# Optimization experiments

Hardware: AMD Instinct MI355X
Metric: run time of the kernel (lower is better)

The kernel has to match this reference:

```python
import jax, jax.numpy as jnp
import numpy as np

B, L, D, N = 4, 1024, 1024, 16
HD = D // N
DFF = 4 * D
EPS = 1e-5


def _ln(x, g, b):
    m = jnp.mean(x, axis=-1, keepdims=True)
    v = jnp.mean(jnp.square(x - m), axis=-1, keepdims=True)
    return (x - m) * jax.lax.rsqrt(v + EPS) * g + b


def setup_inputs() -> dict:
    key = jax.random.key(0)
    ks = jax.random.split(key, 8)
    s = 0.02
    return {
        "x": jax.random.normal(ks[0], (B, L, D), jnp.float32),
        "decay": jax.random.uniform(ks[1], (N, L, L), jnp.float32),
        "ln1_g": jnp.ones((D,), jnp.float32),
        "ln1_b": jnp.zeros((D,), jnp.float32),
        "proj_W": jax.random.normal(ks[2], (4 * D, D), jnp.float32) * s,
        "proj_b": jnp.zeros((4 * D,), jnp.float32),
        "reto_W": jax.random.normal(ks[3], (D, D), jnp.float32) * s,
        "reto_b": jnp.zeros((D,), jnp.float32),
        "ln2_g": jnp.ones((D,), jnp.float32),
        "ln2_b": jnp.zeros((D,), jnp.float32),
        "ffn1_W": jax.random.normal(ks[4], (DFF, D), jnp.float32) * s,
        "ffn1_b": jnp.zeros((DFF,), jnp.float32),
        "ffn2_W": jax.random.normal(ks[5], (D, DFF), jnp.float32) * s,
        "ffn2_b": jnp.zeros((D,), jnp.float32),
    }


def reference(x, decay, ln1_g, ln1_b, proj_W, proj_b, reto_W, reto_b,
              ln2_g, ln2_b, ffn1_W, ffn1_b, ffn2_W, ffn2_b):
    ln_x = _ln(x, ln1_g, ln1_b)
    p = ln_x @ proj_W.T + proj_b                      # [B, L, 4D]
    q, k, v, xo = jnp.split(p, 4, axis=-1)            # each [B, L, D]

    def heads(t):  # [B, L, D] -> [B, N, L, HD]
        return t.reshape(B, L, N, HD).transpose(0, 2, 1, 3)

    q, k, v = heads(q), heads(k), heads(v)
    scores = jnp.einsum('bnld,bnmd->bnlm', q, k) * decay[None]  # [B,N,L,L]
    ret = jnp.einsum('bnlm,bnmd->bnld', scores, v)              # [B,N,L,HD]
    ret = ret.transpose(0, 2, 1, 3).reshape(B, L, D)
    ret = ret * jax.nn.silu(xo)                                  # gated
    ret = ret @ reto_W.T + reto_b
    x = x + ret
    h = _ln(x, ln2_g, ln2_b)
    h = jax.nn.gelu(h @ ffn1_W.T + ffn1_b, approximate=False) @ ffn2_W.T + ffn2_b
    return x + h
```

## Files before the change

kernel.cpp:

```cpp
#include <hip/hip_runtime.h>


typedef _Float16 f16;
typedef _Float16 f16x8 __attribute__((ext_vector_type(8)));
typedef float floatx4 __attribute__((ext_vector_type(4)));

#define EP_BIAS_F16      0
#define EP_DECAY_F16     1
#define EP_BIAS_GELU_F16 2
#define EP_PARTIAL_F32   3

template <bool F32> struct out_sel { typedef f16 T; };
template <> struct out_sel<true>   { typedef float T; };

__device__ __forceinline__ void gload_lds16(const void* g, void* s) {
    __builtin_amdgcn_global_load_lds(
        (const __attribute__((address_space(1))) unsigned int*)g,
        (__attribute__((address_space(3))) unsigned int*)s, 16, 0, 0);
}

__device__ __forceinline__ float erf_fast(float x) {
    const float ax = fabsf(x);
    const float t  = __builtin_amdgcn_rcpf(1.f + 0.3275911f * ax);
    const float p  = t * (0.254829592f + t * (-0.284496736f + t * (1.421413741f +
                     t * (-1.453152027f + t * 1.061405429f))));
    const float r  = 1.f - p * __expf(-ax * ax);
    return copysignf(r, x);
}

__global__ __launch_bounds__(256, 2) void attn_fused(
    const f16* __restrict__ p, const f16* __restrict__ vT,
    const float* __restrict__ decay, f16* __restrict__ gated)
{
    const int y  = blockIdx.y;
    const int bp = y >> 4, h = y & 15;
    const int m0 = blockIdx.x * 64;

    __shared__ __align__(16) f16 Kb[4][64 * 64];
    __shared__ __align__(16) f16 Vb[4][64 * 64];
    __shared__ __align__(16) f16 Ss[4][16 * 68];

    const int t    = threadIdx.x;
    const int lane = t & 63;
    const int w    = t >> 6;
    const int quad = lane >> 4;
    const int fr   = lane & 15;
    const int wq0  = w * 16;

    const int b0 = bp * 2, b1 = b0 + 1;
    const int z0 = b0 * 16 + h, z1 = z0 + 16;
    const f16*   Qg0 = p + ((size_t)h * 4096 + b0 * 1024 + m0) * 64;
    const f16*   Qg1 = p + ((size_t)h * 4096 + b1 * 1024 + m0) * 64;
    const f16*   Kg0 = p + ((size_t)(16 + h) * 4096 + b0 * 1024) * 64;
    const f16*   Kg1 = p + ((size_t)(16 + h) * 4096 + b1 * 1024) * 64;
    const f16*   Vg0 = vT + (size_t)z0 * 65536;
    const f16*   Vg1 = vT + (size_t)z1 * 65536;
    const f16*   XOg0 = p + ((size_t)(48 + h) * 4096 + b0 * 1024 + m0) * 64;
    const f16*   XOg1 = p + ((size_t)(48 + h) * 4096 + b1 * 1024 + m0) * 64;
    const float* Dg  = decay + (size_t)h * 1048576 + (size_t)m0 * 1024;

    f16x8 q00, q01, q10, q11;
    {
        const size_t qrow = (size_t)(wq0 + fr) * 64;
        q00 = *(const f16x8*)(Qg0 + qrow + (0 * 4 + quad) * 8);
        q01 = *(const f16x8*)(Qg0 + qrow + (1 * 4 + quad) * 8);
        q10 = *(const f16x8*)(Qg1 + qrow + (0 * 4 + quad) * 8);
        q11 = *(const f16x8*)(Qg1 + qrow + (1 * 4 + quad) * 8);
    }

    floatx4 oa0[4] = {}, oa1[4] = {};
    float dA[16], dB[16];

    const float* Dt = Dg + (size_t)(wq0 + quad * 4) * 1024 + fr;

#define DLOAD(dst, jj) { _Pragma("unroll") \
    for (int tn = 0; tn < 4; ++tn) { _Pragma("unroll") \
      for (int r = 0; r < 4; ++r) \
        dst[tn * 4 + r] = Dt[(size_t)r * 1024 + (jj) + tn * 16]; } \
    __builtin_amdgcn_sched_barrier(0); }

#define STAGE(Kgp, Vgp, jj, pb) { _Pragma("unroll") \
    for (int i_ = 0; i_ < 2; ++i_) { \
      const int ci = t + i_ * 256; \
      const int r_ = ci >> 3; \
      const int c_ = ((ci & 7) ^ (r_ & 7)) * 8; \
      gload_lds16((Kgp) + (size_t)(jj) * 64 + r_ * 64 + c_, &Kb[pb][ci * 8]); \
      gload_lds16((Vgp) + (size_t)(jj) * 64 + r_ * 64 + c_, &Vb[pb][ci * 8]); \
    } }

#define VMBAR(N) { asm volatile("s_waitcnt vmcnt(" #N ")" ::: "memory"); \
    __builtin_amdgcn_s_barrier(); __builtin_amdgcn_sched_barrier(0); }

#define STEP(qa, qb, oa, dreg, pb) { \
    floatx4 sa[4] = {}; \
    _Pragma("unroll") \
    for (int kc = 0; kc < 2; ++kc) { \
      const int cc = kc * 4 + quad; \
      f16x8 bf[4]; \
      _Pragma("unroll") \
      for (int tn = 0; tn < 4; ++tn) { \
        const int kv = tn * 16 + fr; \
        bf[tn] = *(const f16x8*)&Kb[pb][(kv * 8 + (cc ^ (kv & 7))) * 8]; \
      } \
      _Pragma("unroll") \
      for (int tn = 0; tn < 4; ++tn) \
        sa[tn] = __builtin_amdgcn_mfma_f32_16x16x32_f16(kc ? (qb) : (qa), bf[tn], sa[tn], 0, 0, 0); \
    } \
    _Pragma("unroll") \
    for (int tn = 0; tn < 4; ++tn) { _Pragma("unroll") \
      for (int r = 0; r < 4; ++r) \
        Ss[w][(quad * 4 + r) * 68 + tn * 16 + fr] = (f16)(sa[tn][r] * dreg[tn * 4 + r]); } \
    _Pragma("unroll") \
    for (int kc = 0; kc < 2; ++kc) { \
      const int cc = kc * 4 + quad; \
      const f16x8 af = *(const f16x8*)&Ss[w][fr * 68 + cc * 8]; \
      f16x8 bf[4]; \
      _Pragma("unroll") \
      for (int tn = 0; tn < 4; ++tn) { \
        const int d = tn * 16 + fr; \
        bf[tn] = *(const f16x8*)&Vb[pb][(d * 8 + (cc ^ (d & 7))) * 8]; \
      } \
      _Pragma("unroll") \
      for (int tn = 0; tn < 4; ++tn) \
        oa[tn] = __builtin_amdgcn_mfma_f32_16x16x32_f16(af, bf[tn], oa[tn], 0, 0, 0); \
    } }

#define EPILOG(oa, XOgp, bq) { \
    _Pragma("unroll") \
    for (int tn = 0; tn < 4; ++tn) { _Pragma("unroll") \
      for (int r = 0; r < 4; ++r) { \
        const int qrow = wq0 + quad * 4 + r; \
        const int d = tn * 16 + fr; \
        float g = (float)XOgp[(size_t)qrow * 64 + d]; \
        g = g * __builtin_amdgcn_rcpf(1.f + __expf(-g)); \
        Ss[w][(quad * 4 + r) * 68 + tn * 16 + fr] = (f16)(oa[tn][r] * g); \
      } } \
    f16* Og = gated + (size_t)((bq) * 1024 + m0 + wq0) * 1024 + h * 64; \
    _Pragma("unroll") \
    for (int i = 0; i < 2; ++i) { \
      const int jj = lane + i * 64; \
      const int rr = jj >> 3; \
      const int cc = jj & 7; \
      const uint2 lo = *(const uint2*)&Ss[w][rr * 68 + cc * 8]; \
      const uint2 hi = *(const uint2*)&Ss[w][rr * 68 + cc * 8 + 4]; \
      uint4 val = make_uint4(lo.x, lo.y, hi.x, hi.y); \
      *(uint4*)(Og + (size_t)rr * 1024 + cc * 8) = val; \
    } }

    DLOAD(dA, 0);
    STAGE(Kg0, Vg0, 0, 0);
    STAGE(Kg1, Vg1, 0, 1);
    VMBAR(4);

    for (int i = 0; i < 7; ++i) {
        const int j1 = i * 128 + 64;
        const int j2 = i * 128 + 128;
        DLOAD(dB, j1);
        STAGE(Kg0, Vg0, j1, 2);
        STEP(q00, q01, oa0, dA, 0);
        VMBAR(4);
        STAGE(Kg1, Vg1, j1, 3);
        STEP(q10, q11, oa1, dA, 1);
        VMBAR(4);
        DLOAD(dA, j2);
        STAGE(Kg0, Vg0, j2, 0);
        STEP(q00, q01, oa0, dB, 2);
        VMBAR(4);
        STAGE(Kg1, Vg1, j2, 1);
        STEP(q10, q11, oa1, dB, 3);
        VMBAR(4);
    }
    {
        DLOAD(dB, 960);
        STAGE(Kg0, Vg0, 960, 2);
        STEP(q00, q01, oa0, dA, 0);
        VMBAR(4);
        STAGE(Kg1, Vg1, 960, 3);
        STEP(q10, q11, oa1, dA, 1);
        VMBAR(4);
        STEP(q00, q01, oa0, dB, 2);
        VMBAR(0);
        STEP(q10, q11, oa1, dB, 3);
    }

    EPILOG(oa0, XOg0, b0);
    EPILOG(oa1, XOg1, b1);

#undef DLOAD
#undef STAGE
#undef VMBAR
#undef STEP
#undef EPILOG
}

template <int BM, int BN, int WM, int WN, int EP, int XSWZ, int PTILED = 0>
__global__ __launch_bounds__(256, 4) void gemm_bt(
    const f16* __restrict__ A, const f16* __restrict__ B, void* __restrict__ Cv,
    int M, int N, int K, int lda, int ldb, int ldc,
    long long sAo, long long sAi, long long sBo, long long sBi,
    long long sCo, long long sCi, int inner,
    int nsplit, int Kc, long long sCk,
    const float* __restrict__ bias,
    const void* __restrict__ aux, long long sXo, long long sXi, int ldaux)
{
    constexpr bool OUT_F32 = (EP == EP_PARTIAL_F32);
    typedef typename out_sel<OUT_F32>::T OutT;
    constexpr int ESIZE       = OUT_F32 ? 4 : 2;
    constexpr int CSTRIDE     = BN + 4;
    constexpr int TILE_BYTES  = (BM + BN) * 64 * 2;
    constexpr int STAGE_BYTES = OUT_F32 ? 0 : BM * CSTRIDE * ESIZE;
    constexpr int SMEM_BYTES  = TILE_BYTES > STAGE_BYTES ? TILE_BYTES : STAGE_BYTES;

    __shared__ __align__(16) char smem[SMEM_BYTES];
    f16*  As = (f16*)smem;
    f16*  Bs = (f16*)(smem + BM * 128);
    OutT* Cs = (OutT*)smem;

    int z = blockIdx.z;
    const int ks = z % nsplit; z /= nsplit;
    const int zo = z / inner, zi = z % inner;
    A += zo * sAo + zi * sAi;
    B += zo * sBo + zi * sBi;
    const long long cOff = (long long)zo * sCo + (long long)zi * sCi + (long long)ks * sCk;
    const long long xOff = (long long)zo * sXo + (long long)zi * sXi;

    int bx = blockIdx.x, by = blockIdx.y;
    if constexpr (XSWZ) {
        const int gx  = gridDim.x;
        const int nb  = gx * gridDim.y;
        const int lin = bx + gx * by;
        const int nlin = (lin & 7) * (nb >> 3) + (lin >> 3);
        bx = nlin % gx;
        by = nlin / gx;
    }
    const int m0 = by * BM;
    const int n0 = bx * BN;

    const int t    = threadIdx.x;
    const int lane = t & 63;
    const int w    = t >> 6;
    const int wm   = (w >> 1) * (WM * 16);
    const int wn   = (w & 1) * (WN * 16);
    const int fr   = lane & 15;
    const int quad = lane >> 4;

    constexpr int ACH = BM / 32;
    constexpr int BCH = BN / 32;

    floatx4 acc[WM][WN] = {};

    const int kbeg = ks * Kc, kend = kbeg + Kc;
    for (int kk = kbeg; kk < kend; kk += 64) {
#pragma unroll
        for (int i = 0; i < ACH; ++i) {
            const int ci = t + i * 256;
            const int r  = ci >> 3;
            const int c  = ((ci & 7) ^ (r & 7)) * 8;
            gload_lds16(A + (size_t)(m0 + r) * lda + kk + c, &As[ci * 8]);
        }
#pragma unroll
        for (int i = 0; i < BCH; ++i) {
            const int ci = t + i * 256;
            const int r  = ci >> 3;
            const int c  = ((ci & 7) ^ (r & 7)) * 8;
            gload_lds16(B + (size_t)(n0 + r) * ldb + kk + c, &Bs[ci * 8]);
        }
        __syncthreads();

#pragma unroll
        for (int kh = 0; kh < 2; ++kh) {
            const int cc = kh * 4 + quad;
            f16x8 af[WM], bf[WN];
#pragma unroll
            for (int tm = 0; tm < WM; ++tm) {
                const int r = wm + tm * 16 + fr;
                af[tm] = *(const f16x8*)&As[(r * 8 + (cc ^ (r & 7))) * 8];
            }
#pragma unroll
            for (int tn = 0; tn < WN; ++tn) {
                const int r = wn + tn * 16 + fr;
                bf[tn] = *(const f16x8*)&Bs[(r * 8 + (cc ^ (r & 7))) * 8];
            }
#pragma unroll
            for (int tm = 0; tm < WM; ++tm)
#pragma unroll
                for (int tn = 0; tn < WN; ++tn)
                    acc[tm][tn] = __builtin_amdgcn_mfma_f32_16x16x32_f16(af[tm], bf[tn], acc[tm][tn], 0, 0, 0);
        }
        __syncthreads();
    }

    const int er = quad * 4;
    const int ec = lane & 15;
    if constexpr (OUT_F32) {
        float* Pg = (float*)Cv + cOff;
#pragma unroll
        for (int tm = 0; tm < WM; ++tm)
#pragma unroll
            for (int tn = 0; tn < WN; ++tn)
#pragma unroll
                for (int r = 0; r < 4; ++r) {
                    const int grow = m0 + wm + tm * 16 + er + r;
                    const int gcol = n0 + wn + tn * 16 + ec;
                    Pg[(size_t)grow * ldc + gcol] = acc[tm][tn][r];
                }
        return;
    }

#pragma unroll
    for (int tm = 0; tm < WM; ++tm) {
#pragma unroll
        for (int tn = 0; tn < WN; ++tn) {
#pragma unroll
            for (int r = 0; r < 4; ++r) {
                const int lrow = wm + tm * 16 + er + r;
                const int col  = wn + tn * 16 + ec;
                const int grow = m0 + lrow;
                const int gcol = n0 + col;
                const float v = acc[tm][tn][r];
                float val;
                if constexpr (EP == EP_BIAS_F16) {
                    val = v + bias[gcol];
                } else if constexpr (EP == EP_DECAY_F16) {
                    const float* dk = (const float*)aux + xOff;
                    val = v * dk[(size_t)grow * ldaux + gcol];
                } else if constexpr (EP == EP_BIAS_GELU_F16) {
                    const float u = v + bias[gcol];
                    val = 0.5f * u * (1.f + erf_fast(u * 0.70710678118f));
                } else {
                    val = v;
                }
                Cs[lrow * CSTRIDE + col] = (OutT)val;
            }
        }
    }
    __syncthreads();

    constexpr int PER_ROW = BN * ESIZE / 16;
    constexpr int NCHUNK  = (BM * PER_ROW) / 256;
#pragma unroll
    for (int i = 0; i < NCHUNK; ++i) {
        const int j  = t + i * 256;
        const int rr = j / PER_ROW;
        const int cc = j - rr * PER_ROW;
        const char* src = smem + (size_t)rr * (CSTRIDE * ESIZE) + (size_t)cc * 16;
        const uint2 lo = *(const uint2*)src;
        const uint2 hi = *(const uint2*)(src + 8);
        uint4 val = make_uint4(lo.x, lo.y, hi.x, hi.y);
        char* dst;
        if constexpr (PTILED) {
            const int gc0 = n0 + cc * 8;
            dst = (char*)Cv +
                (((size_t)(gc0 >> 6) * 4096 + (m0 + rr)) * 64 + (gc0 & 63)) * 2;
        } else {
            dst = (char*)Cv +
                (size_t)(cOff + (long long)(m0 + rr) * ldc + n0) * ESIZE +
                (size_t)cc * 16;
        }
        *(uint4*)dst = val;
    }
}

__global__ __launch_bounds__(256) void reduce2_bias_res(
    const float4* __restrict__ P, const float* __restrict__ bias,
    const float4* __restrict__ res, float4* __restrict__ out)
{
    const int i = blockIdx.x * 256 + threadIdx.x;
    const int col4 = i & 255;
    const float4 a = P[i];
    const float4 b = P[i + 1048576];
    const float4 r = res[i];
    const float4 bi = ((const float4*)bias)[col4];
    float4 o;
    o.x = a.x + b.x + r.x + bi.x;
    o.y = a.y + b.y + r.y + bi.y;
    o.z = a.z + b.z + r.z + bi.z;
    o.w = a.w + b.w + r.w + bi.w;
    out[i] = o;
}

__global__ __launch_bounds__(256) void ln_to_f16(
    const float* __restrict__ x, const float* __restrict__ g,
    const float* __restrict__ b, f16* __restrict__ out)
{
    const int row = blockIdx.x;
    const int t = threadIdx.x;
    const float4 xv = ((const float4*)(x + (size_t)row * 1024))[t];
    float s  = xv.x + xv.y + xv.z + xv.w;
    float ss = xv.x * xv.x + xv.y * xv.y + xv.z * xv.z + xv.w * xv.w;
    for (int o = 32; o > 0; o >>= 1) {
        s  += __shfl_down(s, o, 64);
        ss += __shfl_down(ss, o, 64);
    }
    __shared__ float red[8];
    const int wv = t >> 6;
    if ((t & 63) == 0) { red[wv] = s; red[wv + 4] = ss; }
    __syncthreads();
    s  = red[0] + red[1] + red[2] + red[3];
    ss = red[4] + red[5] + red[6] + red[7];
    const float mean = s * (1.f / 1024.f);
    const float var  = ss * (1.f / 1024.f) - mean * mean;
    const float rstd = rsqrtf(var + 1e-5f);
    const float4 gv = ((const float4*)g)[t];
    const float4 bv = ((const float4*)b)[t];
    alignas(8) f16 h[4];
    h[0] = (f16)((xv.x - mean) * rstd * gv.x + bv.x);
    h[1] = (f16)((xv.y - mean) * rstd * gv.y + bv.y);
    h[2] = (f16)((xv.z - mean) * rstd * gv.z + bv.z);
    h[3] = (f16)((xv.w - mean) * rstd * gv.w + bv.w);
    ((uint2*)(out + (size_t)row * 1024))[t] = *(uint2*)h;
}

__global__ __launch_bounds__(256) void cast_f32_f16(
    const float* __restrict__ in, f16* __restrict__ out, int n4)
{
    const int i = blockIdx.x * 256 + threadIdx.x;
    if (i < n4) {
        const float4 v = ((const float4*)in)[i];
        alignas(8) f16 h[4] = {(f16)v.x, (f16)v.y, (f16)v.z, (f16)v.w};
        ((uint2*)out)[i] = *(uint2*)h;
    }
}

__global__ __launch_bounds__(256) void transpose_v(
    const f16* __restrict__ p, f16* __restrict__ vT)
{
    const int z = blockIdx.y;
    const int b = z >> 4, h = z & 15;
    const int m0 = blockIdx.x * 64;
    __shared__ f16 tile[64][72];
    const int t = threadIdx.x;
    const f16* src = p + ((size_t)(32 + h) * 4096 + b * 1024 + m0) * 64;
#pragma unroll
    for (int pass = 0; pass < 4; ++pass) {
        const int r = (t >> 4) + pass * 16;
        const int c = (t & 15) * 4;
        *(uint2*)&tile[r][c] = *(const uint2*)(src + (size_t)r * 64 + c);
    }
    __syncthreads();
    f16* dst = vT + (size_t)z * 65536 + (size_t)(m0 >> 6) * 4096;
#pragma unroll
    for (int pass = 0; pass < 4; ++pass) {
        const int d  = (t >> 4) + pass * 16;
        const int mc = (t & 15) * 4;
        alignas(8) f16 tmp[4] = {tile[mc][d], tile[mc + 1][d], tile[mc + 2][d], tile[mc + 3][d]};
        *(uint2*)(dst + (size_t)d * 64 + mc) = *(uint2*)tmp;
    }
}

extern "C" void kernel_launch(void* const* d_in, const int* in_sizes, int n_in,
                              void* d_out, int out_size, void* d_ws, size_t ws_size,
                              hipStream_t stream) {
    const float* x      = (const float*)d_in[0];
    const float* decay  = (const float*)d_in[1];
    const float* ln1_g  = (const float*)d_in[2];
    const float* ln1_b  = (const float*)d_in[3];
    const float* proj_W = (const float*)d_in[4];
    const float* proj_b = (const float*)d_in[5];
    const float* reto_W = (const float*)d_in[6];
    const float* reto_b = (const float*)d_in[7];
    const float* ln2_g  = (const float*)d_in[8];
    const float* ln2_b  = (const float*)d_in[9];
    const float* ffn1_W = (const float*)d_in[10];
    const float* ffn1_b = (const float*)d_in[11];
    const float* ffn2_W = (const float*)d_in[12];
    const float* ffn2_b = (const float*)d_in[13];
    float* out = (float*)d_out;

    char* w = (char*)d_ws;
    auto alloc = [&](size_t bytes) { char* r = w; w += (bytes + 255) & ~(size_t)255; return r; };
    f16*   Wp   = (f16*)alloc((size_t)4096 * 1024 * 2);
    f16*   Wr   = (f16*)alloc((size_t)1024 * 1024 * 2);
    f16*   W1   = (f16*)alloc((size_t)4096 * 1024 * 2);
    f16*   W2   = (f16*)alloc((size_t)1024 * 4096 * 2);
    f16*   buf8 = (f16*)alloc((size_t)4096 * 1024 * 2);
    f16*   p    = (f16*)alloc((size_t)4096 * 4096 * 2);
    f16*   S    = (f16*)alloc((size_t)16 * 1024 * 1024 * 2);
    float* y    = (float*)alloc((size_t)4096 * 1024 * 4);

    f16*   lnx   = buf8;
    f16*   vT    = buf8;
    f16*   hln   = buf8;
    f16*   gated = Wp;
    f16*   ffh   = p;
    float* Pk    = (float*)S;

    cast_f32_f16<<<4096, 256, 0, stream>>>(proj_W, Wp, 1048576);
    cast_f32_f16<<<1024, 256, 0, stream>>>(reto_W, Wr, 262144);
    cast_f32_f16<<<4096, 256, 0, stream>>>(ffn1_W, W1, 1048576);
    cast_f32_f16<<<4096, 256, 0, stream>>>(ffn2_W, W2, 1048576);

    ln_to_f16<<<4096, 256, 0, stream>>>(x, ln1_g, ln1_b, lnx);

    gemm_bt<128, 128, 4, 4, EP_BIAS_F16, 1, 1><<<dim3(32, 32, 1), 256, 0, stream>>>(
        lnx, Wp, p, 4096, 4096, 1024, 1024, 1024, 4096,
        0, 0, 0, 0, 0, 0, 1, 1, 1024, 0, proj_b, nullptr, 0, 0, 0);

    transpose_v<<<dim3(16, 64), 256, 0, stream>>>(p, vT);

    attn_fused<<<dim3(16, 32), 256, 0, stream>>>(p, vT, decay, gated);

    gemm_bt<128, 128, 4, 4, EP_PARTIAL_F32, 1><<<dim3(8, 32, 2), 256, 0, stream>>>(
        gated, Wr, Pk, 4096, 1024, 1024, 1024, 1024, 1024,
        0, 0, 0, 0, 0, 0, 1, 2, 512, 4194304, nullptr, nullptr, 0, 0, 0);
    reduce2_bias_res<<<4096, 256, 0, stream>>>(
        (const float4*)Pk, reto_b, (const float4*)x, (float4*)y);

    ln_to_f16<<<4096, 256, 0, stream>>>(y, ln2_g, ln2_b, hln);

    gemm_bt<128, 128, 4, 4, EP_BIAS_GELU_F16, 1><<<dim3(32, 32, 1), 256, 0, stream>>>(
        hln, W1, ffh, 4096, 4096, 1024, 1024, 1024, 4096,
        0, 0, 0, 0, 0, 0, 1, 1, 1024, 0, ffn1_b, nullptr, 0, 0, 0);

    gemm_bt<128, 128, 4, 4, EP_PARTIAL_F32, 1><<<dim3(8, 32, 2), 256, 0, stream>>>(
        ffh, W2, Pk, 4096, 1024, 4096, 4096, 4096, 1024,
        0, 0, 0, 0, 0, 0, 1, 2, 2048, 4194304, nullptr, nullptr, 0, 0, 0);
    reduce2_bias_res<<<4096, 256, 0, stream>>>(
        (const float4*)Pk, ffn2_b, (const float4*)y, (float4*)out);
}
```

Baseline: 390.8 us.

## Widen attention blocks to 128 queries with triple-buffered shared K/V tiles

The retention attention kernel now runs 512 threads per block and covers 128 query rows per block instead of 64, so each staged K/V tile in LDS serves eight waves. Global and L2 traffic for K and V drops accordingly. Staging moves from a four-slot ping-pong to a three-stage ring that loads both batches' K/V together, which needs one barrier per step instead of two. The grid halves and each CU holds one large block using about 113KB of LDS rather than two smaller ones. That makes load imbalance across CUs and latency hiding within a single block the main risks.

```diff
diff --git a/kernel.cpp b/kernel.cpp
--- a/kernel.cpp
+++ b/kernel.cpp
@@ -28,17 +28,17 @@
     return copysignf(r, x);
 }
 
-__global__ __launch_bounds__(256, 2) void attn_fused(
+__global__ __launch_bounds__(512, 1) void attn_fused(
     const f16* __restrict__ p, const f16* __restrict__ vT,
     const float* __restrict__ decay, f16* __restrict__ gated)
 {
     const int y  = blockIdx.y;
     const int bp = y >> 4, h = y & 15;
-    const int m0 = blockIdx.x * 64;
-
-    __shared__ __align__(16) f16 Kb[4][64 * 64];
-    __shared__ __align__(16) f16 Vb[4][64 * 64];
-    __shared__ __align__(16) f16 Ss[4][16 * 68];
+    const int m0 = blockIdx.x * 128;
+
+    __shared__ __align__(16) f16 Kb[3][2][64 * 64];
+    __shared__ __align__(16) f16 Vb[3][2][64 * 64];
+    __shared__ __align__(16) f16 Ss[8][16 * 68];
 
     const int t    = threadIdx.x;
     const int lane = t & 63;
@@ -57,7 +57,6 @@
     const f16*   Vg1 = vT + (size_t)z1 * 65536;
     const f16*   XOg0 = p + ((size_t)(48 + h) * 4096 + b0 * 1024 + m0) * 64;
     const f16*   XOg1 = p + ((size_t)(48 + h) * 4096 + b1 * 1024 + m0) * 64;
-    const float* Dg  = decay + (size_t)h * 1048576 + (size_t)m0 * 1024;
 
     f16x8 q00, q01, q10, q11;
     {
@@ -71,7 +70,8 @@
     floatx4 oa0[4] = {}, oa1[4] = {};
     float dA[16], dB[16];
 
-    const float* Dt = Dg + (size_t)(wq0 + quad * 4) * 1024 + fr;
+    const float* Dt = decay + (size_t)h * 1048576
+                    + (size_t)(m0 + wq0 + quad * 4) * 1024 + fr;
 
 #define DLOAD(dst, jj) { _Pragma("unroll") \
     for (int tn = 0; tn < 4; ++tn) { _Pragma("unroll") \
@@ -79,19 +79,19 @@
         dst[tn * 4 + r] = Dt[(size_t)r * 1024 + (jj) + tn * 16]; } \
     __builtin_amdgcn_sched_barrier(0); }
 
-#define STAGE(Kgp, Vgp, jj, pb) { _Pragma("unroll") \
-    for (int i_ = 0; i_ < 2; ++i_) { \
-      const int ci = t + i_ * 256; \
-      const int r_ = ci >> 3; \
-      const int c_ = ((ci & 7) ^ (r_ & 7)) * 8; \
-      gload_lds16((Kgp) + (size_t)(jj) * 64 + r_ * 64 + c_, &Kb[pb][ci * 8]); \
-      gload_lds16((Vgp) + (size_t)(jj) * 64 + r_ * 64 + c_, &Vb[pb][ci * 8]); \
-    } }
+#define STAGE2(jj, pb) { \
+    const int r_ = t >> 3; \
+    const int c_ = ((t & 7) ^ (r_ & 7)) * 8; \
+    const size_t go_ = (size_t)(jj) * 64 + r_ * 64 + c_; \
+    gload_lds16(Kg0 + go_, &Kb[pb][0][t * 8]); \
+    gload_lds16(Vg0 + go_, &Vb[pb][0][t * 8]); \
+    gload_lds16(Kg1 + go_, &Kb[pb][1][t * 8]); \
+    gload_lds16(Vg1 + go_, &Vb[pb][1][t * 8]); }
 
 #define VMBAR(N) { asm volatile("s_waitcnt vmcnt(" #N ")" ::: "memory"); \
     __builtin_amdgcn_s_barrier(); __builtin_amdgcn_sched_barrier(0); }
 
-#define STEP(qa, qb, oa, dreg, pb) { \
+#define STEPB(qa, qb, oa, dreg, kb, vb) { \
     floatx4 sa[4] = {}; \
     _Pragma("unroll") \
     for (int kc = 0; kc < 2; ++kc) { \
@@ -100,7 +100,7 @@
       _Pragma("unroll") \
       for (int tn = 0; tn < 4; ++tn) { \
         const int kv = tn * 16 + fr; \
-        bf[tn] = *(const f16x8*)&Kb[pb][(kv * 8 + (cc ^ (kv & 7))) * 8]; \
+        bf[tn] = *(const f16x8*)&(kb)[(kv * 8 + (cc ^ (kv & 7))) * 8]; \
       } \
       _Pragma("unroll") \
       for (int tn = 0; tn < 4; ++tn) \
@@ -118,7 +118,7 @@
       _Pragma("unroll") \
       for (int tn = 0; tn < 4; ++tn) { \
         const int d = tn * 16 + fr; \
-        bf[tn] = *(const f16x8*)&Vb[pb][(d * 8 + (cc ^ (d & 7))) * 8]; \
+        bf[tn] = *(const f16x8*)&(vb)[(d * 8 + (cc ^ (d & 7))) * 8]; \
       } \
       _Pragma("unroll") \
       for (int tn = 0; tn < 4; ++tn) \
@@ -147,50 +147,48 @@
       *(uint4*)(Og + (size_t)rr * 1024 + cc * 8) = val; \
     } }
 
+#define MSTEP(pb, dcur, dnxt, jnext, jstage) { \
+    DLOAD(dnxt, jnext); \
+    STAGE2(jstage, (pb + 2) % 3); \
+    STEPB(q00, q01, oa0, dcur, Kb[pb][0], Vb[pb][0]); \
+    STEPB(q10, q11, oa1, dcur, Kb[pb][1], Vb[pb][1]); \
+    VMBAR(4); }
+
     DLOAD(dA, 0);
-    STAGE(Kg0, Vg0, 0, 0);
-    STAGE(Kg1, Vg1, 0, 1);
+    STAGE2(0, 0);
+    STAGE2(64, 1);
     VMBAR(4);
 
-    for (int i = 0; i < 7; ++i) {
-        const int j1 = i * 128 + 64;
-        const int j2 = i * 128 + 128;
-        DLOAD(dB, j1);
-        STAGE(Kg0, Vg0, j1, 2);
-        STEP(q00, q01, oa0, dA, 0);
-        VMBAR(4);
-        STAGE(Kg1, Vg1, j1, 3);
-        STEP(q10, q11, oa1, dA, 1);
-        VMBAR(4);
-        DLOAD(dA, j2);
-        STAGE(Kg0, Vg0, j2, 0);
-        STEP(q00, q01, oa0, dB, 2);
-        VMBAR(4);
-        STAGE(Kg1, Vg1, j2, 1);
-        STEP(q10, q11, oa1, dB, 3);
-        VMBAR(4);
-    }
+#pragma unroll
+    for (int i = 0; i < 2; ++i) {
+        const int j0 = i * 384;
+        MSTEP(0, dA, dB, j0 + 64,  j0 + 128);
+        MSTEP(1, dB, dA, j0 + 128, j0 + 192);
+        MSTEP(2, dA, dB, j0 + 192, j0 + 256);
+        MSTEP(0, dB, dA, j0 + 256, j0 + 320);
+        MSTEP(1, dA, dB, j0 + 320, j0 + 384);
+        MSTEP(2, dB, dA, j0 + 384, j0 + 448);
+    }
+    MSTEP(0, dA, dB, 832, 896);
+    MSTEP(1, dB, dA, 896, 960);
     {
         DLOAD(dB, 960);
-        STAGE(Kg0, Vg0, 960, 2);
-        STEP(q00, q01, oa0, dA, 0);
-        VMBAR(4);
-        STAGE(Kg1, Vg1, 960, 3);
-        STEP(q10, q11, oa1, dA, 1);
-        VMBAR(4);
-        STEP(q00, q01, oa0, dB, 2);
+        STEPB(q00, q01, oa0, dA, Kb[2][0], Vb[2][0]);
+        STEPB(q10, q11, oa1, dA, Kb[2][1], Vb[2][1]);
         VMBAR(0);
-        STEP(q10, q11, oa1, dB, 3);
-    }
+    }
+    STEPB(q00, q01, oa0, dB, Kb[0][0], Vb[0][0]);
+    STEPB(q10, q11, oa1, dB, Kb[0][1], Vb[0][1]);
 
     EPILOG(oa0, XOg0, b0);
     EPILOG(oa1, XOg1, b1);
 
 #undef DLOAD
-#undef STAGE
+#undef STAGE2
 #undef VMBAR
-#undef STEP
+#undef STEPB
 #undef EPILOG
+#undef MSTEP
 }
 
 template <int BM, int BN, int WM, int WN, int EP, int XSWZ, int PTILED = 0>
@@ -498,7 +496,7 @@
 
     transpose_v<<<dim3(16, 64), 256, 0, stream>>>(p, vT);
 
-    attn_fused<<<dim3(16, 32), 256, 0, stream>>>(p, vT, decay, gated);
+    attn_fused<<<dim3(8, 32), 512, 0, stream>>>(p, vT, decay, gated);
 
     gemm_bt<128, 128, 4, 4, EP_PARTIAL_F32, 1><<<dim3(8, 32, 2), 256, 0, stream>>>(
         gated, Wr, Pk, 4096, 1024, 1024, 1024, 1024, 1024,
```

New measurement: 398.6 us. Within noise of the previous version (+2.0%).
